# Optimization experiments

Hardware: AMD Instinct MI355X
Metric: run time of the kernel (lower is better)

## Reference

```python
import jax, jax.numpy as jnp
import numpy as np

# Config (matches init_kwargs)
N, P, K, DIMS = 16, 1024, 16, 3
C_IN, C_MID, C_OUT, DM = 64, 64, 128, 4
C_CAT = C_MID + C_IN          # channels entering depthwise-separable conv
KK = K * K
BN_EPS = 1e-5


def setup_inputs() -> dict:
    key = jax.random.key(0)
    ks = jax.random.split(key, 24)
    s = 0.05  # small init scale for weights
    inp = {
        # forward args
        "rep_pt": jax.random.normal(ks[0], (N, P, DIMS), jnp.float32),
        "pts":    jax.random.normal(ks[1], (N, P, K, DIMS), jnp.float32),
        "fts":    jax.random.normal(ks[2], (N, P, K, C_IN), jnp.float32),
        # dense1 / dense2 (point lifting MLP), weights stored (in, out)
        "w1": jax.random.normal(ks[3], (DIMS, C_MID), jnp.float32) * s,
        "b1": jnp.zeros((C_MID,), jnp.float32),
        "w2": jax.random.normal(ks[4], (C_MID, C_MID), jnp.float32) * s,
        "b2": jnp.zeros((C_MID,), jnp.float32),
        # conv1: Conv2d(dims, K*K, (1,K)); weight (KK, dims, K)
        "wc1": jax.random.normal(ks[5], (KK, DIMS, K), jnp.float32) * s,
        "bc1": jnp.zeros((KK,), jnp.float32),
        # x_dense1 (ELU) and x_dense2 (no activation)
        "wx1": jax.random.normal(ks[6], (KK, KK), jnp.float32) * s,
        "bx1": jnp.zeros((KK,), jnp.float32),
        "wx2": jax.random.normal(ks[7], (KK, KK), jnp.float32) * s,
        "bx2": jnp.zeros((KK,), jnp.float32),
        # depthwise Conv2d(C_CAT, C_CAT*DM, (1,K), groups=C_CAT): weight (C_CAT, DM, K)
        "wdw": jax.random.normal(ks[8], (C_CAT, DM, K), jnp.float32) * s,
        "bdw": jnp.zeros((C_CAT * DM,), jnp.float32),
        # pointwise Conv2d(C_CAT*DM, C_OUT, 1): weight stored (C_CAT*DM, C_OUT)
        "wpw": jax.random.normal(ks[9], (C_CAT * DM, C_OUT), jnp.float32) * s,
        "bpw": jnp.zeros((C_OUT,), jnp.float32),
        # BatchNorm2d(C_OUT) in eval mode (running stats)
        "bn_gamma": jnp.ones((C_OUT,), jnp.float32),
        "bn_beta":  jnp.zeros((C_OUT,), jnp.float32),
        "bn_mean":  jax.random.normal(ks[10], (C_OUT,), jnp.float32) * 0.1,
        "bn_var":   jax.random.uniform(ks[11], (C_OUT,), jnp.float32, 0.5, 1.5),
    }
    return inp


def reference(rep_pt, pts, fts, w1, b1, w2, b2, wc1, bc1, wx1, bx1, wx2, bx2,
              wdw, bdw, wpw, bpw, bn_gamma, bn_beta, bn_mean, bn_var):
    elu = jax.nn.elu
    n, p, k = pts.shape[0], pts.shape[1], pts.shape[2]

    # localize points around representative point: (N,P,K,dims)
    pts_local = pts - rep_pt[:, :, None, :]

    # lift coordinates to C_mid features (two Dense+ELU)
    h = elu(pts_local @ w1 + b1)
    h = elu(h @ w2 + b2)
    fts_cat = jnp.concatenate([h, fts], axis=-1)  # (N,P,K,C_CAT)

    # learned X-transform: conv1 over the K neighbors -> (N,P,K*K)
    X = elu(jnp.einsum('npkd,odk->npo', pts_local, wc1) + bc1)
    X = elu(X @ wx1 + bx1)
    X = X @ wx2 + bx2            # x_dense2: no activation
    X = X.reshape(n, p, k, k)    # (N,P,K,K)

    # apply X-transform to concatenated features
    fts_X = jnp.einsum('npij,npjc->npic', X, fts_cat)  # (N,P,K,C_CAT)

    # depthwise conv (kernel (1,K), groups=C_CAT, depth multiplier DM)
    # torch grouped-conv channel order: out channel o = c*DM + d
    dw = jnp.einsum('npkc,cdk->npcd', fts_X, wdw).reshape(n, p, -1) + bdw
    # pointwise 1x1 conv -> C_OUT, then ELU
    y = elu(dw @ wpw + bpw)      # (N,P,C_OUT)
    # BatchNorm2d in eval mode (per-channel affine with running stats)
    y = (y - bn_mean) * (bn_gamma / jnp.sqrt(bn_var + BN_EPS)) + bn_beta
    return y                     # (N,P,C_OUT)
```

## Files before the change

### kernel.cpp

```cpp
#include <hip/hip_runtime.h>

#define NPTS 16384
#define MPB  16
#define NTHR 512
#define WS_NEEDED 401408u

typedef __attribute__((ext_vector_type(8))) short bf16x8;
typedef __attribute__((ext_vector_type(4))) float f32x4;

__device__ __forceinline__ unsigned short f2bf(float x) {
    unsigned u = __float_as_uint(x);
    return (unsigned short)((u + 0x7FFFu + ((u >> 16) & 1u)) >> 16);
}
__device__ __forceinline__ unsigned pk2(float a, float b) {
    return (unsigned)f2bf(a) | ((unsigned)f2bf(b) << 16);
}
__device__ __forceinline__ float bf2f(unsigned short h) {
    return __uint_as_float(((unsigned)h) << 16);
}
__device__ __forceinline__ float elu_f(float x) {
    return x > 0.f ? x : (__expf(x) - 1.f);
}

__device__ __forceinline__ bf16x8 load_bfrag(const float* __restrict__ W, int N,
                                             int kt, int nt, int lane) {
    int k0  = kt * 32 + ((lane >> 4) << 3);
    int col = nt * 16 + (lane & 15);
    const float* s = W + k0 * N + col;
    bf16x8 r;
#pragma unroll
    for (int j = 0; j < 8; j++) r[j] = (short)f2bf(s[j * N]);
    return r;
}

__global__ void pack_weights(const float* __restrict__ w2,
                             const float* __restrict__ wx1,
                             const float* __restrict__ wx2,
                             const float* __restrict__ wpw,
                             unsigned short* __restrict__ dst) {
    int gid  = blockIdx.x * 256 + threadIdx.x;
    int frag = gid >> 6, lane = gid & 63;
    const float* src; int N, fl;
    if      (frag <   8) { src = w2;  N =  64; fl = frag;       }
    else if (frag < 136) { src = wx1; N = 256; fl = frag - 8;   }
    else if (frag < 264) { src = wx2; N = 256; fl = frag - 136; }
    else                 { src = wpw; N = 128; fl = frag - 264; }
    int NT  = N >> 4;
    int kt  = fl / NT, nt = fl - kt * NT;
    int k0  = kt * 32 + (lane >> 4) * 8;
    int col = nt * 16 + (lane & 15);
    const float* s = src + k0 * N + col;
    unsigned v[4];
#pragma unroll
    for (int u = 0; u < 4; u++) {
        unsigned lo = f2bf(s[(2 * u) * N]);
        unsigned hi = f2bf(s[(2 * u + 1) * N]);
        v[u] = lo | (hi << 16);
    }
    *(uint4*)&dst[gid * 8] = make_uint4(v[0], v[1], v[2], v[3]);
}

template <bool PACKED>
__global__ __launch_bounds__(NTHR, 2)
void xconv_main(const float* __restrict__ rep_pt, const float* __restrict__ pts,
                const float* __restrict__ fts,
                const float* __restrict__ w1,  const float* __restrict__ b1,
                const float* __restrict__ w2,  const float* __restrict__ b2,
                const float* __restrict__ wc1, const float* __restrict__ bc1,
                const float* __restrict__ wx1, const float* __restrict__ bx1,
                const float* __restrict__ wx2, const float* __restrict__ bx2,
                const float* __restrict__ wdw, const float* __restrict__ bdw,
                const float* __restrict__ wpw, const float* __restrict__ bpw,
                const float* __restrict__ bn_gamma, const float* __restrict__ bn_beta,
                const float* __restrict__ bn_mean,  const float* __restrict__ bn_var,
                const unsigned short* __restrict__ wpack,
                float* __restrict__ out) {
    __shared__ __align__(16) char smem[60928];
    float*          s_ptsl = (float*)smem;
    unsigned short* s_h2f  = (unsigned short*)(smem + 3072);
    unsigned short* s_x0   = (unsigned short*)(smem + 35840);
    unsigned short* s_x2f  = (unsigned short*)(smem + 35840);
    unsigned short* s_x1   = (unsigned short*)(smem + 44288);
    unsigned short* s_dw   = (unsigned short*)(smem + 44288);

    const int t    = threadIdx.x;
    const int lane = t & 63;
    const int w    = t >> 6;
    const int cl   = lane & 15;
    const int hh   = lane >> 4;
    const int gp0  = blockIdx.x * MPB;

    for (int idx = t; idx < MPB * 48; idx += NTHR) {
        int m = idx / 48, r = idx - m * 48;
        int k = r / 3,    d = r - k * 3;
        int gp = gp0 + m;
        s_ptsl[idx] = pts[(gp * 16 + k) * 3 + d] - rep_pt[gp * 3 + d];
    }
    __syncthreads();

    if (w >= 4) {
        const bf16x8* wp = (const bf16x8*)wpack;
        float w1s[2][3][8], b1s[2][8];
#pragma unroll
        for (int kt = 0; kt < 2; kt++) {
#pragma unroll
            for (int d = 0; d < 3; d++)
#pragma unroll
                for (int j = 0; j < 8; j++)
                    w1s[kt][d][j] = w1[d * 64 + kt * 32 + hh * 8 + j];
#pragma unroll
            for (int j = 0; j < 8; j++) b1s[kt][j] = b1[kt * 32 + hh * 8 + j];
        }
        bf16x8 af[4][2];
#pragma unroll
        for (int i = 0; i < 4; i++) {
            int tile = (w - 4) * 4 + i;
            float p0 = s_ptsl[tile * 48 + cl * 3 + 0];
            float p1 = s_ptsl[tile * 48 + cl * 3 + 1];
            float p2 = s_ptsl[tile * 48 + cl * 3 + 2];
#pragma unroll
            for (int kt = 0; kt < 2; kt++) {
                unsigned v[4];
#pragma unroll
                for (int u = 0; u < 4; u++) {
                    int j0 = 2 * u, j1 = 2 * u + 1;
                    float ha = elu_f(fmaf(p0, w1s[kt][0][j0],
                                     fmaf(p1, w1s[kt][1][j0],
                                     fmaf(p2, w1s[kt][2][j0], b1s[kt][j0]))));
                    float hb = elu_f(fmaf(p0, w1s[kt][0][j1],
                                     fmaf(p1, w1s[kt][1][j1],
                                     fmaf(p2, w1s[kt][2][j1], b1s[kt][j1]))));
                    v[u] = pk2(ha, hb);
                }
                union { bf16x8 b8; uint4 u4; } ua;
                ua.u4 = make_uint4(v[0], v[1], v[2], v[3]);
                af[i][kt] = ua.b8;
            }
        }
        float bias[4];
#pragma unroll
        for (int nt = 0; nt < 4; nt++) bias[nt] = b2[nt * 16 + cl];
#pragma unroll
        for (int nt = 0; nt < 4; nt++) {
            bf16x8 b0, b1f;
            if (PACKED) { b0 = wp[(0 * 4 + nt) * 64 + lane]; b1f = wp[(1 * 4 + nt) * 64 + lane]; }
            else        { b0 = load_bfrag(w2, 64, 0, nt, lane); b1f = load_bfrag(w2, 64, 1, nt, lane); }
#pragma unroll
            for (int i = 0; i < 4; i++) {
                int tile = (w - 4) * 4 + i;
                f32x4 acc = {bias[nt], bias[nt], bias[nt], bias[nt]};
                acc = __builtin_amdgcn_mfma_f32_16x16x32_bf16(af[i][0], b0,  acc, 0, 0, 0);
                acc = __builtin_amdgcn_mfma_f32_16x16x32_bf16(af[i][1], b1f, acc, 0, 0, 0);
                unsigned lo = pk2(elu_f(acc[0]), elu_f(acc[1]));
                unsigned hi = pk2(elu_f(acc[2]), elu_f(acc[3]));
                unsigned short* dp = &s_h2f[(((tile * 4 + nt) * 32) + (hh >> 1) * 16 + cl) * 8 + (hh & 1) * 4];
                *(uint2*)dp = make_uint2(lo, hi);
            }
        }
    } else {
        float wreg[48];
#pragma unroll
        for (int q = 0; q < 12; q++) {
            float4 wv = *(const float4*)&wc1[t * 48 + q * 4];
            wreg[q * 4 + 0] = wv.x; wreg[q * 4 + 1] = wv.y;
            wreg[q * 4 + 2] = wv.z; wreg[q * 4 + 3] = wv.w;
        }
        float bo = bc1[t];
#pragma unroll 1
        for (int m = 0; m < MPB; m++) {
            float acc = bo;
#pragma unroll
            for (int q = 0; q < 12; q++) {
                float4 pv = *(const float4*)&s_ptsl[m * 48 + q * 4];
                acc = fmaf(pv.x, wreg[((q * 4 + 0) % 3) * 16 + (q * 4 + 0) / 3], acc);
                acc = fmaf(pv.y, wreg[((q * 4 + 1) % 3) * 16 + (q * 4 + 1) / 3], acc);
                acc = fmaf(pv.z, wreg[((q * 4 + 2) % 3) * 16 + (q * 4 + 2) / 3], acc);
                acc = fmaf(pv.w, wreg[((q * 4 + 3) % 3) * 16 + (q * 4 + 3) / 3], acc);
            }
            s_x0[m * 264 + t] = f2bf(elu_f(acc));
        }
    }
    __syncthreads();

    {
        const bf16x8* wp = (const bf16x8*)wpack + 512;
        bf16x8 A[8];
#pragma unroll
        for (int kt = 0; kt < 8; kt++)
            A[kt] = *(const bf16x8*)&s_x0[cl * 264 + kt * 32 + hh * 8];
        f32x4 acc[2];
#pragma unroll
        for (int q = 0; q < 2; q++) {
            float bv = bx1[(w * 2 + q) * 16 + cl];
            acc[q] = (f32x4){bv, bv, bv, bv};
        }
#pragma unroll
        for (int kb = 0; kb < 2; kb++) {
            bf16x8 B0[4], B1[4];
#pragma unroll
            for (int j = 0; j < 4; j++) {
                int kt = kb * 4 + j;
                if (PACKED) { B0[j] = wp[(kt * 16 + w * 2 + 0) * 64 + lane];
                              B1[j] = wp[(kt * 16 + w * 2 + 1) * 64 + lane]; }
                else        { B0[j] = load_bfrag(wx1, 256, kt, w * 2 + 0, lane);
                              B1[j] = load_bfrag(wx1, 256, kt, w * 2 + 1, lane); }
            }
#pragma unroll
            for (int j = 0; j < 4; j++) {
                acc[0] = __builtin_amdgcn_mfma_f32_16x16x32_bf16(A[kb * 4 + j], B0[j], acc[0], 0, 0, 0);
                acc[1] = __builtin_amdgcn_mfma_f32_16x16x32_bf16(A[kb * 4 + j], B1[j], acc[1], 0, 0, 0);
            }
        }
#pragma unroll
        for (int q = 0; q < 2; q++) {
            int nt = w * 2 + q;
#pragma unroll
            for (int r = 0; r < 4; r++) {
                int m = hh * 4 + r;
                s_x1[m * 264 + nt * 16 + cl] = f2bf(elu_f(acc[q][r]));
            }
        }
    }
    __syncthreads();

    {
        const bf16x8* wp = (const bf16x8*)wpack + 8704;
        bf16x8 A[8];
#pragma unroll
        for (int kt = 0; kt < 8; kt++)
            A[kt] = *(const bf16x8*)&s_x1[cl * 264 + kt * 32 + hh * 8];
        f32x4 acc[2];
#pragma unroll
        for (int q = 0; q < 2; q++) {
            float bv = bx2[(w * 2 + q) * 16 + cl];
            acc[q] = (f32x4){bv, bv, bv, bv};
        }
#pragma unroll
        for (int kb = 0; kb < 2; kb++) {
            bf16x8 B0[4], B1[4];
#pragma unroll
            for (int j = 0; j < 4; j++) {
                int kt = kb * 4 + j;
                if (PACKED) { B0[j] = wp[(kt * 16 + w * 2 + 0) * 64 + lane];
                              B1[j] = wp[(kt * 16 + w * 2 + 1) * 64 + lane]; }
                else        { B0[j] = load_bfrag(wx2, 256, kt, w * 2 + 0, lane);
                              B1[j] = load_bfrag(wx2, 256, kt, w * 2 + 1, lane); }
            }
#pragma unroll
            for (int j = 0; j < 4; j++) {
                acc[0] = __builtin_amdgcn_mfma_f32_16x16x32_bf16(A[kb * 4 + j], B0[j], acc[0], 0, 0, 0);
                acc[1] = __builtin_amdgcn_mfma_f32_16x16x32_bf16(A[kb * 4 + j], B1[j], acc[1], 0, 0, 0);
            }
        }
#pragma unroll
        for (int q = 0; q < 2; q++) {
            int ntE = w * 2 + q;
            int lp  = (cl >> 3) * 16 + ntE;
            int jj  = cl & 7;
#pragma unroll
            for (int r = 0; r < 4; r++) {
                int m = hh * 4 + r;
                s_x2f[(m * 32 + lp) * 8 + jj] = f2bf(acc[q][r]);
            }
        }
    }
    __syncthreads();

    {
        const int  cH    = (w & 3) * 16 + cl;
        const bool isF   = (w >= 4);
        const int  cFull = isF ? (64 + cH) : cH;
        float wd[16];
#pragma unroll
        for (int d = 0; d < 4; d++) {
            float4 v = *(const float4*)&wdw[cFull * 64 + d * 16 + 4 * hh];
            wd[d * 4 + 0] = v.x; wd[d * 4 + 1] = v.y;
            wd[d * 4 + 2] = v.z; wd[d * 4 + 3] = v.w;
        }
        float4 bd = *(const float4*)&bdw[cFull * 4];
        const float* ftsp = fts + (size_t)gp0 * 1024 + cH;

        float f0[8], f1[8], f2[8], f3[8];
        auto LDF = [&](int m, float* f) {
            if (isF && lane < 32) {
                const float* p = ftsp + (m * 16 + hh * 8) * 64;
#pragma unroll
                for (int j = 0; j < 8; j++) f[j] = p[j * 64];
            }
        };
        auto STEP = [&](int m, float* fc_, float* fl_) {
            if (m + 3 < 16) LDF(m + 3, fl_);
            bf16x8 a = {};
            if (lane < 32) a = *(const bf16x8*)&s_x2f[(m * 32 + lane) * 8];
            bf16x8 b = {};
            if (isF) {
                if (lane < 32) {
                    union { bf16x8 v; uint4 u; } ub;
                    ub.u = make_uint4(pk2(fc_[0], fc_[1]), pk2(fc_[2], fc_[3]),
                                      pk2(fc_[4], fc_[5]), pk2(fc_[6], fc_[7]));
                    b = ub.v;
                }
            } else {
                if (lane < 32) b = *(const bf16x8*)&s_h2f[((m * 4 + (w & 3)) * 32 + lane) * 8];
            }
            f32x4 acc = {0.f, 0.f, 0.f, 0.f};
            acc = __builtin_amdgcn_mfma_f32_16x16x32_bf16(a, b, acc, 0, 0, 0);
            float o[4];
#pragma unroll
            for (int d = 0; d < 4; d++) {
                float s = acc[0] * wd[d * 4 + 0];
                s = fmaf(acc[1], wd[d * 4 + 1], s);
                s = fmaf(acc[2], wd[d * 4 + 2], s);
                s = fmaf(acc[3], wd[d * 4 + 3], s);
                s += __shfl_xor(s, 16);
                s += __shfl_xor(s, 32);
                o[d] = s;
            }
            if (hh == 0) {
                ushort4 v;
                v.x = f2bf(o[0] + bd.x); v.y = f2bf(o[1] + bd.y);
                v.z = f2bf(o[2] + bd.z); v.w = f2bf(o[3] + bd.w);
                *(ushort4*)&s_dw[m * 520 + cFull * 4] = v;
            }
        };
        LDF(0, f0); LDF(1, f1); LDF(2, f2);
#pragma unroll
        for (int q = 0; q < 4; q++) {
            STEP(4 * q + 0, f0, f3);
            STEP(4 * q + 1, f1, f0);
            STEP(4 * q + 2, f2, f1);
            STEP(4 * q + 3, f3, f2);
        }
    }
    __syncthreads();

    {
        const bf16x8* wp = (const bf16x8*)wpack + 16896;
        float bv = bpw[w * 16 + cl];
        f32x4 acc = {bv, bv, bv, bv};
#pragma unroll
        for (int kb = 0; kb < 2; kb++) {
            bf16x8 A[8], B[8];
#pragma unroll
            for (int j = 0; j < 8; j++) {
                int kt = kb * 8 + j;
                if (PACKED) B[j] = wp[(kt * 8 + w) * 64 + lane];
                else        B[j] = load_bfrag(wpw, 128, kt, w, lane);
                A[j] = *(const bf16x8*)&s_dw[cl * 520 + kt * 32 + hh * 8];
            }
#pragma unroll
            for (int j = 0; j < 8; j++)
                acc = __builtin_amdgcn_mfma_f32_16x16x32_bf16(A[j], B[j], acc, 0, 0, 0);
        }
        int co = w * 16 + cl;
        float scale = bn_gamma[co] * rsqrtf(bn_var[co] + 1e-5f);
        float shift = bn_beta[co] - bn_mean[co] * scale;
#pragma unroll
        for (int r = 0; r < 4; r++) {
            int m = hh * 4 + r;
            out[(gp0 + m) * 128 + co] = fmaf(elu_f(acc[r]), scale, shift);
        }
    }
}

extern "C" void kernel_launch(void* const* d_in, const int* in_sizes, int n_in,
                              void* d_out, int out_size, void* d_ws, size_t ws_size,
                              hipStream_t stream) {
    const float* rep_pt   = (const float*)d_in[0];
    const float* pts      = (const float*)d_in[1];
    const float* fts      = (const float*)d_in[2];
    const float* w1       = (const float*)d_in[3];
    const float* b1       = (const float*)d_in[4];
    const float* w2       = (const float*)d_in[5];
    const float* b2       = (const float*)d_in[6];
    const float* wc1      = (const float*)d_in[7];
    const float* bc1      = (const float*)d_in[8];
    const float* wx1      = (const float*)d_in[9];
    const float* bx1      = (const float*)d_in[10];
    const float* wx2      = (const float*)d_in[11];
    const float* bx2      = (const float*)d_in[12];
    const float* wdw      = (const float*)d_in[13];
    const float* bdw      = (const float*)d_in[14];
    const float* wpw      = (const float*)d_in[15];
    const float* bpw      = (const float*)d_in[16];
    const float* bn_gamma = (const float*)d_in[17];
    const float* bn_beta  = (const float*)d_in[18];
    const float* bn_mean  = (const float*)d_in[19];
    const float* bn_var   = (const float*)d_in[20];
    float* out = (float*)d_out;

    const bool packed = (d_ws != nullptr) && (ws_size >= (size_t)WS_NEEDED);
    unsigned short* wpack = (unsigned short*)d_ws;

    if (packed) {
        pack_weights<<<98, 256, 0, stream>>>(w2, wx1, wx2, wpw, wpack);
        xconv_main<true><<<NPTS / MPB, NTHR, 0, stream>>>(
            rep_pt, pts, fts, w1, b1, w2, b2, wc1, bc1, wx1, bx1, wx2, bx2,
            wdw, bdw, wpw, bpw, bn_gamma, bn_beta, bn_mean, bn_var, wpack, out);
    } else {
        xconv_main<false><<<NPTS / MPB, NTHR, 0, stream>>>(
            rep_pt, pts, fts, w1, b1, w2, b2, wc1, bc1, wx1, bx1, wx2, bx2,
            wdw, bdw, wpw, bpw, bn_gamma, bn_beta, bn_mean, bn_var, (const unsigned short*)nullptr, out);
    }
}
```

Before: 185.8 us.

## Move conv1 X-transform to MFMA with split-bf16 inputs and rebalance warps

```diff
diff --git a/kernel.cpp b/kernel.cpp
--- a/kernel.cpp
+++ b/kernel.cpp
@@ -3,7 +3,7 @@
 #define NPTS 16384
 #define MPB  16
 #define NTHR 512
-#define WS_NEEDED 401408u
+#define WS_NEEDED 434176u
 
 typedef __attribute__((ext_vector_type(8))) short bf16x8;
 typedef __attribute__((ext_vector_type(4))) float f32x4;
@@ -37,9 +37,24 @@
                              const float* __restrict__ wx1,
                              const float* __restrict__ wx2,
                              const float* __restrict__ wpw,
+                             const float* __restrict__ wc1,
                              unsigned short* __restrict__ dst) {
     int gid  = blockIdx.x * 256 + threadIdx.x;
     int frag = gid >> 6, lane = gid & 63;
+    unsigned v[4];
+    if (frag >= 392) {
+        int fl = frag - 392, kt = fl >> 4, nt = fl & 15;
+        int col = nt * 16 + (lane & 15);
+#pragma unroll
+        for (int u = 0; u < 4; u++) {
+            int f0 = kt * 32 + (lane >> 4) * 8 + 2 * u;
+            float a = (f0     < 48) ? wc1[col * 48 + (f0 % 3) * 16 + (f0 / 3)] : 0.f;
+            float b = (f0 + 1 < 48) ? wc1[col * 48 + ((f0 + 1) % 3) * 16 + ((f0 + 1) / 3)] : 0.f;
+            v[u] = pk2(a, b);
+        }
+        *(uint4*)&dst[gid * 8] = make_uint4(v[0], v[1], v[2], v[3]);
+        return;
+    }
     const float* src; int N, fl;
     if      (frag <   8) { src = w2;  N =  64; fl = frag;       }
     else if (frag < 136) { src = wx1; N = 256; fl = frag - 8;   }
@@ -50,7 +65,6 @@
     int k0  = kt * 32 + (lane >> 4) * 8;
     int col = nt * 16 + (lane & 15);
     const float* s = src + k0 * N + col;
-    unsigned v[4];
 #pragma unroll
     for (int u = 0; u < 4; u++) {
         unsigned lo = f2bf(s[(2 * u) * N]);
@@ -98,7 +112,68 @@
     }
     __syncthreads();
 
-    if (w >= 4) {
+    {
+        const bf16x8* wpc = (const bf16x8*)wpack + 25088;
+        const float* pr = &s_ptsl[cl * 48];
+        bf16x8 A0h, A0l, A1h, A1l;
+        {
+            unsigned vh[4], vl[4];
+#pragma unroll
+            for (int u = 0; u < 4; u++) {
+                float a = pr[hh * 8 + 2 * u], b = pr[hh * 8 + 2 * u + 1];
+                unsigned short ah = f2bf(a), bh = f2bf(b);
+                vh[u] = (unsigned)ah | ((unsigned)bh << 16);
+                vl[u] = pk2(a - bf2f(ah), b - bf2f(bh));
+            }
+            union { bf16x8 b8; uint4 u4; } ua;
+            ua.u4 = make_uint4(vh[0], vh[1], vh[2], vh[3]); A0h = ua.b8;
+            ua.u4 = make_uint4(vl[0], vl[1], vl[2], vl[3]); A0l = ua.b8;
+            if (hh < 2) {
+#pragma unroll
+                for (int u = 0; u < 4; u++) {
+                    float a = pr[32 + hh * 8 + 2 * u], b = pr[32 + hh * 8 + 2 * u + 1];
+                    unsigned short ah = f2bf(a), bh = f2bf(b);
+                    vh[u] = (unsigned)ah | ((unsigned)bh << 16);
+                    vl[u] = pk2(a - bf2f(ah), b - bf2f(bh));
+                }
+            } else {
+#pragma unroll
+                for (int u = 0; u < 4; u++) { vh[u] = 0u; vl[u] = 0u; }
+            }
+            ua.u4 = make_uint4(vh[0], vh[1], vh[2], vh[3]); A1h = ua.b8;
+            ua.u4 = make_uint4(vl[0], vl[1], vl[2], vl[3]); A1l = ua.b8;
+        }
+        auto ld_wc1 = [&](int kt, int nt) -> bf16x8 {
+            bf16x8 r;
+#pragma unroll
+            for (int j = 0; j < 8; j++) {
+                int f = kt * 32 + hh * 8 + j;
+                int col = nt * 16 + cl;
+                r[j] = (f < 48) ? (short)f2bf(wc1[col * 48 + (f % 3) * 16 + (f / 3)]) : (short)0;
+            }
+            return r;
+        };
+#pragma unroll
+        for (int q = 0; q < 2; q++) {
+            int nt = w * 2 + q;
+            bf16x8 B0, B1;
+            if (PACKED) { B0 = wpc[(0 * 16 + nt) * 64 + lane]; B1 = wpc[(1 * 16 + nt) * 64 + lane]; }
+            else        { B0 = ld_wc1(0, nt);                  B1 = ld_wc1(1, nt); }
+            float bv = bc1[nt * 16 + cl];
+            f32x4 acc = {bv, bv, bv, bv};
+            acc = __builtin_amdgcn_mfma_f32_16x16x32_bf16(A0l, B0, acc, 0, 0, 0);
+            acc = __builtin_amdgcn_mfma_f32_16x16x32_bf16(A1l, B1, acc, 0, 0, 0);
+            acc = __builtin_amdgcn_mfma_f32_16x16x32_bf16(A0h, B0, acc, 0, 0, 0);
+            acc = __builtin_amdgcn_mfma_f32_16x16x32_bf16(A1h, B1, acc, 0, 0, 0);
+#pragma unroll
+            for (int r = 0; r < 4; r++) {
+                int m = hh * 4 + r;
+                s_x0[m * 264 + nt * 16 + cl] = f2bf(elu_f(acc[r]));
+            }
+        }
+    }
+
+    {
         const bf16x8* wp = (const bf16x8*)wpack;
         float w1s[2][3][8], b1s[2][8];
 #pragma unroll
@@ -111,10 +186,10 @@
 #pragma unroll
             for (int j = 0; j < 8; j++) b1s[kt][j] = b1[kt * 32 + hh * 8 + j];
         }
-        bf16x8 af[4][2];
-#pragma unroll
-        for (int i = 0; i < 4; i++) {
-            int tile = (w - 4) * 4 + i;
+        bf16x8 af[2][2];
+#pragma unroll
+        for (int i = 0; i < 2; i++) {
+            int tile = w * 2 + i;
             float p0 = s_ptsl[tile * 48 + cl * 3 + 0];
             float p1 = s_ptsl[tile * 48 + cl * 3 + 1];
             float p2 = s_ptsl[tile * 48 + cl * 3 + 2];
@@ -142,42 +217,20 @@
         for (int nt = 0; nt < 4; nt++) bias[nt] = b2[nt * 16 + cl];
 #pragma unroll
         for (int nt = 0; nt < 4; nt++) {
-            bf16x8 b0, b1f;
-            if (PACKED) { b0 = wp[(0 * 4 + nt) * 64 + lane]; b1f = wp[(1 * 4 + nt) * 64 + lane]; }
-            else        { b0 = load_bfrag(w2, 64, 0, nt, lane); b1f = load_bfrag(w2, 64, 1, nt, lane); }
-#pragma unroll
-            for (int i = 0; i < 4; i++) {
-                int tile = (w - 4) * 4 + i;
+            bf16x8 bA, bB;
+            if (PACKED) { bA = wp[(0 * 4 + nt) * 64 + lane]; bB = wp[(1 * 4 + nt) * 64 + lane]; }
+            else        { bA = load_bfrag(w2, 64, 0, nt, lane); bB = load_bfrag(w2, 64, 1, nt, lane); }
+#pragma unroll
+            for (int i = 0; i < 2; i++) {
+                int tile = w * 2 + i;
                 f32x4 acc = {bias[nt], bias[nt], bias[nt], bias[nt]};
-                acc = __builtin_amdgcn_mfma_f32_16x16x32_bf16(af[i][0], b0,  acc, 0, 0, 0);
-                acc = __builtin_amdgcn_mfma_f32_16x16x32_bf16(af[i][1], b1f, acc, 0, 0, 0);
+                acc = __builtin_amdgcn_mfma_f32_16x16x32_bf16(af[i][0], bA, acc, 0, 0, 0);
+                acc = __builtin_amdgcn_mfma_f32_16x16x32_bf16(af[i][1], bB, acc, 0, 0, 0);
                 unsigned lo = pk2(elu_f(acc[0]), elu_f(acc[1]));
                 unsigned hi = pk2(elu_f(acc[2]), elu_f(acc[3]));
                 unsigned short* dp = &s_h2f[(((tile * 4 + nt) * 32) + (hh >> 1) * 16 + cl) * 8 + (hh & 1) * 4];
                 *(uint2*)dp = make_uint2(lo, hi);
             }
-        }
-    } else {
-        float wreg[48];
-#pragma unroll
-        for (int q = 0; q < 12; q++) {
-            float4 wv = *(const float4*)&wc1[t * 48 + q * 4];
-            wreg[q * 4 + 0] = wv.x; wreg[q * 4 + 1] = wv.y;
-            wreg[q * 4 + 2] = wv.z; wreg[q * 4 + 3] = wv.w;
-        }
-        float bo = bc1[t];
-#pragma unroll 1
-        for (int m = 0; m < MPB; m++) {
-            float acc = bo;
-#pragma unroll
-            for (int q = 0; q < 12; q++) {
-                float4 pv = *(const float4*)&s_ptsl[m * 48 + q * 4];
-                acc = fmaf(pv.x, wreg[((q * 4 + 0) % 3) * 16 + (q * 4 + 0) / 3], acc);
-                acc = fmaf(pv.y, wreg[((q * 4 + 1) % 3) * 16 + (q * 4 + 1) / 3], acc);
-                acc = fmaf(pv.z, wreg[((q * 4 + 2) % 3) * 16 + (q * 4 + 2) / 3], acc);
-                acc = fmaf(pv.w, wreg[((q * 4 + 3) % 3) * 16 + (q * 4 + 3) / 3], acc);
-            }
-            s_x0[m * 264 + t] = f2bf(elu_f(acc));
         }
     }
     __syncthreads();
@@ -270,6 +323,8 @@
         const int  cH    = (w & 3) * 16 + cl;
         const bool isF   = (w >= 4);
         const int  cFull = isF ? (64 + cH) : cH;
+        const int  o1    = hh & 1, o2 = (hh >> 1) & 1;
+        const int  dfin  = o1 * 2 + o2;
         float wd[16];
 #pragma unroll
         for (int d = 0; d < 4; d++) {
@@ -277,7 +332,7 @@
             wd[d * 4 + 0] = v.x; wd[d * 4 + 1] = v.y;
             wd[d * 4 + 2] = v.z; wd[d * 4 + 3] = v.w;
         }
-        float4 bd = *(const float4*)&bdw[cFull * 4];
+        float bdl = bdw[cFull * 4 + dfin];
         const float* ftsp = fts + (size_t)gp0 * 1024 + cH;
 
         float f0[8], f1[8], f2[8], f3[8];
@@ -305,23 +360,25 @@
             }
             f32x4 acc = {0.f, 0.f, 0.f, 0.f};
             acc = __builtin_amdgcn_mfma_f32_16x16x32_bf16(a, b, acc, 0, 0, 0);
-            float o[4];
+            float p[4];
 #pragma unroll
             for (int d = 0; d < 4; d++) {
                 float s = acc[0] * wd[d * 4 + 0];
                 s = fmaf(acc[1], wd[d * 4 + 1], s);
                 s = fmaf(acc[2], wd[d * 4 + 2], s);
                 s = fmaf(acc[3], wd[d * 4 + 3], s);
-                s += __shfl_xor(s, 16);
-                s += __shfl_xor(s, 32);
-                o[d] = s;
-            }
-            if (hh == 0) {
-                ushort4 v;
-                v.x = f2bf(o[0] + bd.x); v.y = f2bf(o[1] + bd.y);
-                v.z = f2bf(o[2] + bd.z); v.w = f2bf(o[3] + bd.w);
-                *(ushort4*)&s_dw[m * 520 + cFull * 4] = v;
-            }
+                p[d] = s;
+            }
+            float u  = o1 ? p[0] : p[2];
+            float v  = o1 ? p[1] : p[3];
+            float us = __shfl_xor(u, 16);
+            float vs = __shfl_xor(v, 16);
+            float s0 = (o1 ? p[2] : p[0]) + us;
+            float s1 = (o1 ? p[3] : p[1]) + vs;
+            float x  = o2 ? s0 : s1;
+            float xs = __shfl_xor(x, 32);
+            float dv = (o2 ? s1 : s0) + xs;
+            s_dw[m * 520 + cFull * 4 + dfin] = f2bf(dv + bdl);
         };
         LDF(0, f0); LDF(1, f1); LDF(2, f2);
 #pragma unroll
@@ -393,7 +450,7 @@
     unsigned short* wpack = (unsigned short*)d_ws;
 
     if (packed) {
-        pack_weights<<<98, 256, 0, stream>>>(w2, wx1, wx2, wpw, wpack);
+        pack_weights<<<106, 256, 0, stream>>>(w2, wx1, wx2, wpw, wc1, wpack);
         xconv_main<true><<<NPTS / MPB, NTHR, 0, stream>>>(
             rep_pt, pts, fts, w1, b1, w2, b2, wc1, bc1, wx1, bx1, wx2, bx2,
             wdw, bdw, wpw, bpw, bn_gamma, bn_beta, bn_mean, bn_var, wpack, out);
```

New measurement: 180.2 us. 3.0% less time.
